# Kernel tuning notes

Hardware: AMD Instinct MI355X
Metric: run time of the kernel (lower is better)

## Reference

```python
import jax, jax.numpy as jnp
import numpy as np

B, S, D = 4, 4096, 128

def setup_inputs() -> dict:
    key = jax.random.key(0)
    kx, kq, kk, kv = jax.random.split(key, 4)
    x = jax.random.normal(kx, (B, S, D), dtype=jnp.float32)
    Wq = jax.random.normal(kq, (D, D), dtype=jnp.float32) * (1.0 / np.sqrt(D))
    Wk = jax.random.normal(kk, (D, D), dtype=jnp.float32) * (1.0 / np.sqrt(D))
    Wv = jax.random.normal(kv, (D, D), dtype=jnp.float32) * (1.0 / np.sqrt(D))
    return {"x": x, "Wq": Wq, "Wk": Wk, "Wv": Wv}

def reference(x, Wq, Wk, Wv):
    b, s, d = x.shape
    # nn.Linear(bias=False): y = x @ W.T
    q = jnp.einsum('bsd,ed->bse', x, Wq)
    k = jnp.einsum('bsd,ed->bse', x, Wk)
    v = jnp.einsum('bsd,ed->bse', x, Wv)
    scores = jnp.einsum('bqd,bkd->bqk', q, k) / jnp.sqrt(jnp.float32(d))
    causal = jnp.tril(jnp.ones((s, s), dtype=bool))  # [s,s]
    scores = jnp.where(causal, scores, jnp.float32(-jnp.inf))
    weights = jax.nn.softmax(scores.astype(jnp.float32), axis=-1)
    out = jnp.einsum('bqk,bkd->bqd', weights, v)
    return out  # dropout is identity in eval / p=0
```

## Files before the change

kernel.cpp:

```cpp
#include <hip/hip_runtime.h>
#include <hip/hip_bf16.h>
#include <math.h>

typedef __attribute__((ext_vector_type(8))) short short8;
typedef __attribute__((ext_vector_type(4))) float f32x4;
typedef __attribute__((ext_vector_type(4))) float float4v;
typedef __attribute__((ext_vector_type(4))) unsigned short ushort4v;

#define B_ 4
#define S_ 4096
#define D_ 128

#define CHUNKS_PER_BATCH 288
#define NSLOT (B_ * CHUNKS_PER_BATCH)

__device__ __forceinline__ unsigned short f2bf(float f) {
    union { float f; unsigned u; } v; v.f = f;
    unsigned r = v.u + 0x7FFFu + ((v.u >> 16) & 1u);
    return (unsigned short)(r >> 16);
}
__device__ __forceinline__ float bf2f(unsigned short h) {
    union { unsigned u; float f; } v; v.u = ((unsigned)h) << 16;
    return v.f;
}

__global__ void wconv_kernel(const float* __restrict__ Wq,
                             const float* __restrict__ Wk,
                             const float* __restrict__ Wv,
                             unsigned short* __restrict__ Wb) {
    int i = blockIdx.x * 256 + threadIdx.x;
    if (i >= 3 * 16384) return;
    const float* s = (i < 16384) ? Wq : (i < 32768 ? Wk : Wv);
    Wb[i] = f2bf(s[i & 16383]);
}

__global__ __launch_bounds__(256) void qkv_kernel(const float* __restrict__ X,
                                                  const unsigned short* __restrict__ Wb,
                                                  unsigned short* __restrict__ Qb,
                                                  unsigned short* __restrict__ Kb,
                                                  unsigned short* __restrict__ Vt) {
    __shared__ __align__(16) unsigned short Xb[64 * 128];
    const int tid = threadIdx.x;
    const int r0 = blockIdx.x * 64;
    const int grp = blockIdx.y;

    const float4v* src = reinterpret_cast<const float4v*>(X + (long)r0 * 128);
    #pragma unroll
    for (int it = 0; it < 8; ++it) {
        int idx = it * 256 + tid;
        float4v v = src[idx];
        ushort4v p;
        p[0] = f2bf(v[0]); p[1] = f2bf(v[1]); p[2] = f2bf(v[2]); p[3] = f2bf(v[3]);
        *reinterpret_cast<ushort4v*>(&Xb[idx * 4]) = p;
    }
    __syncthreads();

    const int lane = tid & 63, w = tid >> 6;
    const int l16 = lane & 15, g = lane >> 4;

    short8 a[4];
    #pragma unroll
    for (int kb = 0; kb < 4; ++kb)
        a[kb] = *reinterpret_cast<const short8*>(&Xb[(w * 16 + l16) * 128 + kb * 32 + g * 8]);

    #pragma unroll
    for (int ct = 0; ct < 8; ++ct) {
        const int e = ct * 16 + l16;
        const int c = grp * 128 + e;
        f32x4 acc = {0.f, 0.f, 0.f, 0.f};
        #pragma unroll
        for (int kb = 0; kb < 4; ++kb) {
            short8 bf = *reinterpret_cast<const short8*>(Wb + (long)c * 128 + kb * 32 + g * 8);
            acc = __builtin_amdgcn_mfma_f32_16x16x32_bf16(a[kb], bf, acc, 0, 0, 0);
        }
        const int row0 = r0 + w * 16 + g * 4;
        if (grp == 0) {
            #pragma unroll
            for (int r = 0; r < 4; ++r) Qb[(long)(row0 + r) * 128 + e] = f2bf(acc[r]);
        } else if (grp == 1) {
            #pragma unroll
            for (int r = 0; r < 4; ++r) Kb[(long)(row0 + r) * 128 + e] = f2bf(acc[r]);
        } else {
            const int bb = row0 >> 12, ss = row0 & 4095;
            ushort4v p;
            p[0] = f2bf(acc[0]); p[1] = f2bf(acc[1]); p[2] = f2bf(acc[2]); p[3] = f2bf(acc[3]);
            *reinterpret_cast<ushort4v*>(&Vt[((long)bb * 128 + e) * 4096 + ss]) = p;
        }
    }
}

__global__ __launch_bounds__(256) void attn_kernel(const unsigned short* __restrict__ Qb,
                                                   const unsigned short* __restrict__ Kb,
                                                   const unsigned short* __restrict__ Vt,
                                                   unsigned short* __restrict__ Opart,
                                                   float* __restrict__ Mpart,
                                                   float* __restrict__ Lpart) {
    __shared__ __align__(16) unsigned char lds[40960];

    const int tid = threadIdx.x;
    const int lane = tid & 63, w = tid >> 6;
    const int l16 = lane & 15, g = lane >> 4;

    const int bidx = (int)blockIdx.x;
    const int b = bidx / CHUNKS_PER_BATCH;
    const int rr = bidx - b * CHUNKS_PER_BATCH;
    int gg = 0;
    while (4 * (gg + 1) * (gg + 2) <= rr) ++gg;
    const int j = rr - 4 * gg * (gg + 1);
    const int qt = 8 * gg + j / (gg + 1);
    const int c = j % (gg + 1);
    const int slot = bidx;

    const unsigned short* Qbase = Qb + (long)b * S_ * D_;
    const unsigned short* Kbase = Kb + (long)b * S_ * D_;
    const unsigned short* Vbase = Vt + (long)b * D_ * S_;

    const int qrow_f = qt * 64 + w * 16 + l16;
    short8 qf[4];
    #pragma unroll
    for (int kb = 0; kb < 4; ++kb)
        qf[kb] = *reinterpret_cast<const short8*>(Qbase + (long)qrow_f * 128 + kb * 32 + g * 8);

    f32x4 o[8];
    #pragma unroll
    for (int dt = 0; dt < 8; ++dt) o[dt] = (f32x4){0.f, 0.f, 0.f, 0.f};
    float m[4], lsum[4];
    int myrow[4];
    #pragma unroll
    for (int r = 0; r < 4; ++r) {
        m[r] = -INFINITY; lsum[r] = 0.f;
        myrow[r] = qt * 64 + w * 16 + g * 4 + r;
    }

    const float scale = 0.08838834764831845f;
    const int kt0 = c * 8;
    const int ktend = min(kt0 + 7, qt);

    for (int kt = kt0; kt <= ktend; ++kt) {
        #pragma unroll
        for (int it = 0; it < 4; ++it) {
            int ch = it * 256 + tid;
            int row = ch >> 4, cd = ch & 15;
            short8 vk = *reinterpret_cast<const short8*>(Kbase + (long)(kt * 64 + row) * 128 + cd * 8);
            int byt = (row * 256 + cd * 16) ^ ((row & 7) << 4);
            *reinterpret_cast<short8*>(lds + byt) = vk;

            int rowd = ch >> 3, ckv = ch & 7;
            short8 vv = *reinterpret_cast<const short8*>(Vbase + (long)rowd * 4096 + kt * 64 + ckv * 8);
            int bytv = (rowd * 128 + ckv * 16) ^ ((rowd & 7) << 4);
            *reinterpret_cast<short8*>(lds + 16384 + bytv) = vv;
        }
        __syncthreads();

        f32x4 s[4];
        #pragma unroll
        for (int ct = 0; ct < 4; ++ct) {
            s[ct] = (f32x4){0.f, 0.f, 0.f, 0.f};
            const int kvl = ct * 16 + l16;
            #pragma unroll
            for (int kb = 0; kb < 4; ++kb) {
                int byt = (kvl * 256 + kb * 64 + g * 16) ^ ((kvl & 7) << 4);
                short8 kf = *reinterpret_cast<const short8*>(lds + byt);
                s[ct] = __builtin_amdgcn_mfma_f32_16x16x32_bf16(qf[kb], kf, s[ct], 0, 0, 0);
            }
        }

        const bool diag = (kt == qt);
        float rmax[4] = {-1e30f, -1e30f, -1e30f, -1e30f};
        #pragma unroll
        for (int ct = 0; ct < 4; ++ct) {
            #pragma unroll
            for (int r = 0; r < 4; ++r) {
                float sv = s[ct][r] * scale;
                if (diag && (kt * 64 + ct * 16 + l16 > myrow[r])) sv = -1e30f;
                s[ct][r] = sv;
                rmax[r] = fmaxf(rmax[r], sv);
            }
        }
        #pragma unroll
        for (int off = 1; off < 16; off <<= 1) {
            #pragma unroll
            for (int r = 0; r < 4; ++r) rmax[r] = fmaxf(rmax[r], __shfl_xor(rmax[r], off, 64));
        }
        float al[4], rsum[4];
        #pragma unroll
        for (int r = 0; r < 4; ++r) {
            float mn = fmaxf(m[r], rmax[r]);
            al[r] = __expf(m[r] - mn);
            m[r] = mn;
            rsum[r] = 0.f;
        }
        #pragma unroll
        for (int ct = 0; ct < 4; ++ct) {
            #pragma unroll
            for (int r = 0; r < 4; ++r) {
                float p = __expf(s[ct][r] - m[r]);
                s[ct][r] = p;
                rsum[r] += p;
            }
        }
        #pragma unroll
        for (int off = 1; off < 16; off <<= 1) {
            #pragma unroll
            for (int r = 0; r < 4; ++r) rsum[r] += __shfl_xor(rsum[r], off, 64);
        }
        #pragma unroll
        for (int r = 0; r < 4; ++r) lsum[r] = lsum[r] * al[r] + rsum[r];
        #pragma unroll
        for (int dt = 0; dt < 8; ++dt) {
            #pragma unroll
            for (int r = 0; r < 4; ++r) o[dt][r] *= al[r];
        }

        unsigned char* Pw = lds + 32768 + w * 2048;
        #pragma unroll
        for (int ct = 0; ct < 4; ++ct) {
            #pragma unroll
            for (int r = 0; r < 4; ++r) {
                int pr = g * 4 + r, pc = ct * 16 + l16;
                int byt = (pr * 128 + pc * 2) ^ ((pr & 7) << 4);
                *reinterpret_cast<unsigned short*>(Pw + byt) = f2bf(s[ct][r]);
            }
        }

        #pragma unroll
        for (int kvb = 0; kvb < 2; ++kvb) {
            int pbyt = (l16 * 128 + kvb * 64 + g * 16) ^ ((l16 & 7) << 4);
            short8 pf = *reinterpret_cast<const short8*>(Pw + pbyt);
            #pragma unroll
            for (int dt = 0; dt < 8; ++dt) {
                int d = dt * 16 + l16;
                int vbyt = (d * 128 + kvb * 64 + g * 16) ^ ((d & 7) << 4);
                short8 vf = *reinterpret_cast<const short8*>(lds + 16384 + vbyt);
                o[dt] = __builtin_amdgcn_mfma_f32_16x16x32_bf16(pf, vf, o[dt], 0, 0, 0);
            }
        }
        __syncthreads();
    }

    unsigned short* Op = Opart + (long)slot * 8192;
    #pragma unroll
    for (int dt = 0; dt < 8; ++dt) {
        #pragma unroll
        for (int r = 0; r < 4; ++r) {
            Op[(w * 16 + g * 4 + r) * 128 + dt * 16 + l16] = f2bf(o[dt][r]);
        }
    }
    if (l16 == 0) {
        #pragma unroll
        for (int r = 0; r < 4; ++r) {
            Mpart[(long)slot * 64 + w * 16 + g * 4 + r] = m[r];
            Lpart[(long)slot * 64 + w * 16 + g * 4 + r] = lsum[r];
        }
    }
}

__global__ __launch_bounds__(256) void combine_kernel(const unsigned short* __restrict__ Opart,
                                                      const float* __restrict__ Mpart,
                                                      const float* __restrict__ Lpart,
                                                      float* __restrict__ out) {
    __shared__ float coeff[8][64];
    __shared__ float invL[64];

    const int qt = blockIdx.x, b = blockIdx.y;
    const int gg = qt >> 3;
    const int nc = gg + 1;
    const int slot0 = b * CHUNKS_PER_BATCH + 4 * gg * (gg + 1) + (qt - 8 * gg) * nc;

    const int tid = threadIdx.x;
    if (tid < 64) {
        float mg = -INFINITY;
        for (int c = 0; c < nc; ++c)
            mg = fmaxf(mg, Mpart[(long)(slot0 + c) * 64 + tid]);
        float L = 0.f;
        for (int c = 0; c < nc; ++c) {
            float co = __expf(Mpart[(long)(slot0 + c) * 64 + tid] - mg);
            coeff[c][tid] = co;
            L += co * Lpart[(long)(slot0 + c) * 64 + tid];
        }
        invL[tid] = 1.f / L;
    }
    __syncthreads();

    #pragma unroll
    for (int it = 0; it < 4; ++it) {
        const int e0 = (it * 256 + tid) * 8;
        const int r = e0 >> 7;
        float acc[8];
        #pragma unroll
        for (int k = 0; k < 8; ++k) acc[k] = 0.f;
        for (int c = 0; c < nc; ++c) {
            short8 v = *reinterpret_cast<const short8*>(Opart + (long)(slot0 + c) * 8192 + e0);
            const float co = coeff[c][r];
            #pragma unroll
            for (int k = 0; k < 8; ++k)
                acc[k] += co * bf2f((unsigned short)v[k]);
        }
        const float s = invL[r];
        float4v o0, o1;
        o0[0] = acc[0] * s; o0[1] = acc[1] * s; o0[2] = acc[2] * s; o0[3] = acc[3] * s;
        o1[0] = acc[4] * s; o1[1] = acc[5] * s; o1[2] = acc[6] * s; o1[3] = acc[7] * s;
        float* dst = out + ((long)b * S_ + qt * 64) * 128 + e0;
        *reinterpret_cast<float4v*>(dst) = o0;
        *reinterpret_cast<float4v*>(dst + 4) = o1;
    }
}

extern "C" void kernel_launch(void* const* d_in, const int* in_sizes, int n_in,
                              void* d_out, int out_size, void* d_ws, size_t ws_size,
                              hipStream_t stream) {
    (void)in_sizes; (void)n_in; (void)out_size; (void)ws_size;
    const float* x  = (const float*)d_in[0];
    const float* Wq = (const float*)d_in[1];
    const float* Wk = (const float*)d_in[2];
    const float* Wv = (const float*)d_in[3];
    float* out = (float*)d_out;

    char* ws = (char*)d_ws;
    const size_t MB4 = (size_t)16384 * 128 * 2;
    unsigned short* Qb = (unsigned short*)(ws);
    unsigned short* Kb = (unsigned short*)(ws + MB4);
    unsigned short* Vt = (unsigned short*)(ws + 2 * MB4);
    unsigned short* Wb = (unsigned short*)(ws + 3 * MB4);
    unsigned short* Opart = (unsigned short*)(ws + 3 * MB4 + (1 << 20));
    float* Mpart = (float*)(ws + 3 * MB4 + (1 << 20) + (size_t)NSLOT * 8192 * 2);
    float* Lpart = Mpart + (size_t)NSLOT * 64;

    wconv_kernel<<<192, 256, 0, stream>>>(Wq, Wk, Wv, Wb);
    qkv_kernel<<<dim3(256, 3), 256, 0, stream>>>(x, Wb, Qb, Kb, Vt);
    attn_kernel<<<NSLOT, 256, 0, stream>>>(Qb, Kb, Vt, Opart, Mpart, Lpart);
    combine_kernel<<<dim3(64, 4), 256, 0, stream>>>(Opart, Mpart, Lpart, out);
}
```

Before: 160.0 us.

## Prefetch next K/V tile into registers, drop QKV LDS staging, split combine blocks

The attention kernel now loads the next K/V tile into registers while the current tile's MFMAs run, then writes it to LDS between barriers. It also adds a min-blocks-per-CU launch bound of 3. The QKV projection loads X straight from global into MFMA fragments instead of staging through LDS. The combine kernel is split into four times as many blocks, each covering 16 rows, to raise parallelism. The prefetch adds register pressure and an extra barrier per iteration, and the launch bound may force spills.

```diff
diff --git a/kernel.cpp b/kernel.cpp
--- a/kernel.cpp
+++ b/kernel.cpp
@@ -39,29 +39,30 @@
                                                   unsigned short* __restrict__ Qb,
                                                   unsigned short* __restrict__ Kb,
                                                   unsigned short* __restrict__ Vt) {
-    __shared__ __align__(16) unsigned short Xb[64 * 128];
     const int tid = threadIdx.x;
+    const int lane = tid & 63, w = tid >> 6;
+    const int l16 = lane & 15, g = lane >> 4;
     const int r0 = blockIdx.x * 64;
     const int grp = blockIdx.y;
 
-    const float4v* src = reinterpret_cast<const float4v*>(X + (long)r0 * 128);
-    #pragma unroll
-    for (int it = 0; it < 8; ++it) {
-        int idx = it * 256 + tid;
-        float4v v = src[idx];
-        ushort4v p;
-        p[0] = f2bf(v[0]); p[1] = f2bf(v[1]); p[2] = f2bf(v[2]); p[3] = f2bf(v[3]);
-        *reinterpret_cast<ushort4v*>(&Xb[idx * 4]) = p;
-    }
-    __syncthreads();
-
-    const int lane = tid & 63, w = tid >> 6;
-    const int l16 = lane & 15, g = lane >> 4;
-
+    const int row = r0 + w * 16 + l16;
+    const float* xr = X + (long)row * 128;
+    float4v x0[4], x1[4];
+    #pragma unroll
+    for (int kb = 0; kb < 4; ++kb) {
+        x0[kb] = *reinterpret_cast<const float4v*>(xr + kb * 32 + g * 8);
+        x1[kb] = *reinterpret_cast<const float4v*>(xr + kb * 32 + g * 8 + 4);
+    }
     short8 a[4];
     #pragma unroll
-    for (int kb = 0; kb < 4; ++kb)
-        a[kb] = *reinterpret_cast<const short8*>(&Xb[(w * 16 + l16) * 128 + kb * 32 + g * 8]);
+    for (int kb = 0; kb < 4; ++kb) {
+        short8 t;
+        t[0] = f2bf(x0[kb][0]); t[1] = f2bf(x0[kb][1]);
+        t[2] = f2bf(x0[kb][2]); t[3] = f2bf(x0[kb][3]);
+        t[4] = f2bf(x1[kb][0]); t[5] = f2bf(x1[kb][1]);
+        t[6] = f2bf(x1[kb][2]); t[7] = f2bf(x1[kb][3]);
+        a[kb] = t;
+    }
 
     #pragma unroll
     for (int ct = 0; ct < 8; ++ct) {
@@ -89,12 +90,12 @@
     }
 }
 
-__global__ __launch_bounds__(256) void attn_kernel(const unsigned short* __restrict__ Qb,
-                                                   const unsigned short* __restrict__ Kb,
-                                                   const unsigned short* __restrict__ Vt,
-                                                   unsigned short* __restrict__ Opart,
-                                                   float* __restrict__ Mpart,
-                                                   float* __restrict__ Lpart) {
+__global__ __launch_bounds__(256, 3) void attn_kernel(const unsigned short* __restrict__ Qb,
+                                                      const unsigned short* __restrict__ Kb,
+                                                      const unsigned short* __restrict__ Vt,
+                                                      unsigned short* __restrict__ Opart,
+                                                      float* __restrict__ Mpart,
+                                                      float* __restrict__ Lpart) {
     __shared__ __align__(16) unsigned char lds[40960];
 
     const int tid = threadIdx.x;
@@ -136,21 +137,45 @@
     const int kt0 = c * 8;
     const int ktend = min(kt0 + 7, qt);
 
+    const int kch = tid, krow0 = kch >> 2, kcd = kch & 3;
+    (void)kch; (void)krow0; (void)kcd;
+
+    short8 kR[4], vR[4];
+    int kbyt[4], vbyt[4];
+    const unsigned short* kaddr[4];
+    const unsigned short* vaddr[4];
+    #pragma unroll
+    for (int it = 0; it < 4; ++it) {
+        int ch = it * 256 + tid;
+        int row = ch >> 4, cd = ch & 15;
+        kaddr[it] = Kbase + (long)row * 128 + cd * 8;
+        kbyt[it] = (row * 256 + cd * 16) ^ ((row & 7) << 4);
+        int rowd = ch >> 3, ckv = ch & 7;
+        vaddr[it] = Vbase + (long)rowd * 4096 + ckv * 8;
+        vbyt[it] = 16384 + ((rowd * 128 + ckv * 16) ^ ((rowd & 7) << 4));
+    }
+
+    #pragma unroll
+    for (int it = 0; it < 4; ++it) {
+        kR[it] = *reinterpret_cast<const short8*>(kaddr[it] + (long)kt0 * 64 * 128);
+        vR[it] = *reinterpret_cast<const short8*>(vaddr[it] + kt0 * 64);
+    }
+    #pragma unroll
+    for (int it = 0; it < 4; ++it) {
+        *reinterpret_cast<short8*>(lds + kbyt[it]) = kR[it];
+        *reinterpret_cast<short8*>(lds + vbyt[it]) = vR[it];
+    }
+    __syncthreads();
+
     for (int kt = kt0; kt <= ktend; ++kt) {
-        #pragma unroll
-        for (int it = 0; it < 4; ++it) {
-            int ch = it * 256 + tid;
-            int row = ch >> 4, cd = ch & 15;
-            short8 vk = *reinterpret_cast<const short8*>(Kbase + (long)(kt * 64 + row) * 128 + cd * 8);
-            int byt = (row * 256 + cd * 16) ^ ((row & 7) << 4);
-            *reinterpret_cast<short8*>(lds + byt) = vk;
-
-            int rowd = ch >> 3, ckv = ch & 7;
-            short8 vv = *reinterpret_cast<const short8*>(Vbase + (long)rowd * 4096 + kt * 64 + ckv * 8);
-            int bytv = (rowd * 128 + ckv * 16) ^ ((rowd & 7) << 4);
-            *reinterpret_cast<short8*>(lds + 16384 + bytv) = vv;
-        }
-        __syncthreads();
+        const bool more = (kt < ktend);
+        if (more) {
+            #pragma unroll
+            for (int it = 0; it < 4; ++it) {
+                kR[it] = *reinterpret_cast<const short8*>(kaddr[it] + (long)(kt + 1) * 64 * 128);
+                vR[it] = *reinterpret_cast<const short8*>(vaddr[it] + (kt + 1) * 64);
+            }
+        }
 
         f32x4 s[4];
         #pragma unroll
@@ -230,12 +255,21 @@
             #pragma unroll
             for (int dt = 0; dt < 8; ++dt) {
                 int d = dt * 16 + l16;
-                int vbyt = (d * 128 + kvb * 64 + g * 16) ^ ((d & 7) << 4);
-                short8 vf = *reinterpret_cast<const short8*>(lds + 16384 + vbyt);
+                int vbyt2 = 16384 + ((d * 128 + kvb * 64 + g * 16) ^ ((d & 7) << 4));
+                short8 vf = *reinterpret_cast<const short8*>(lds + vbyt2);
                 o[dt] = __builtin_amdgcn_mfma_f32_16x16x32_bf16(pf, vf, o[dt], 0, 0, 0);
             }
         }
-        __syncthreads();
+
+        if (more) {
+            __syncthreads();
+            #pragma unroll
+            for (int it = 0; it < 4; ++it) {
+                *reinterpret_cast<short8*>(lds + kbyt[it]) = kR[it];
+                *reinterpret_cast<short8*>(lds + vbyt[it]) = vR[it];
+            }
+            __syncthreads();
+        }
     }
 
     unsigned short* Op = Opart + (long)slot * 8192;
@@ -259,51 +293,49 @@
                                                       const float* __restrict__ Mpart,
                                                       const float* __restrict__ Lpart,
                                                       float* __restrict__ out) {
-    __shared__ float coeff[8][64];
-    __shared__ float invL[64];
-
-    const int qt = blockIdx.x, b = blockIdx.y;
+    __shared__ float coeff[8][16];
+    __shared__ float invL[16];
+
+    const int qt = blockIdx.x >> 2, qq = blockIdx.x & 3, b = blockIdx.y;
     const int gg = qt >> 3;
     const int nc = gg + 1;
     const int slot0 = b * CHUNKS_PER_BATCH + 4 * gg * (gg + 1) + (qt - 8 * gg) * nc;
+    const int r0 = qq * 16;
 
     const int tid = threadIdx.x;
-    if (tid < 64) {
+    if (tid < 16) {
         float mg = -INFINITY;
         for (int c = 0; c < nc; ++c)
-            mg = fmaxf(mg, Mpart[(long)(slot0 + c) * 64 + tid]);
+            mg = fmaxf(mg, Mpart[(long)(slot0 + c) * 64 + r0 + tid]);
         float L = 0.f;
         for (int c = 0; c < nc; ++c) {
-            float co = __expf(Mpart[(long)(slot0 + c) * 64 + tid] - mg);
+            float co = __expf(Mpart[(long)(slot0 + c) * 64 + r0 + tid] - mg);
             coeff[c][tid] = co;
-            L += co * Lpart[(long)(slot0 + c) * 64 + tid];
+            L += co * Lpart[(long)(slot0 + c) * 64 + r0 + tid];
         }
         invL[tid] = 1.f / L;
     }
     __syncthreads();
 
-    #pragma unroll
-    for (int it = 0; it < 4; ++it) {
-        const int e0 = (it * 256 + tid) * 8;
-        const int r = e0 >> 7;
-        float acc[8];
-        #pragma unroll
-        for (int k = 0; k < 8; ++k) acc[k] = 0.f;
-        for (int c = 0; c < nc; ++c) {
-            short8 v = *reinterpret_cast<const short8*>(Opart + (long)(slot0 + c) * 8192 + e0);
-            const float co = coeff[c][r];
-            #pragma unroll
-            for (int k = 0; k < 8; ++k)
-                acc[k] += co * bf2f((unsigned short)v[k]);
-        }
-        const float s = invL[r];
-        float4v o0, o1;
-        o0[0] = acc[0] * s; o0[1] = acc[1] * s; o0[2] = acc[2] * s; o0[3] = acc[3] * s;
-        o1[0] = acc[4] * s; o1[1] = acc[5] * s; o1[2] = acc[6] * s; o1[3] = acc[7] * s;
-        float* dst = out + ((long)b * S_ + qt * 64) * 128 + e0;
-        *reinterpret_cast<float4v*>(dst) = o0;
-        *reinterpret_cast<float4v*>(dst + 4) = o1;
-    }
+    const int e0 = tid * 8;
+    const int r = e0 >> 7;
+    float acc[8];
+    #pragma unroll
+    for (int k = 0; k < 8; ++k) acc[k] = 0.f;
+    for (int c = 0; c < nc; ++c) {
+        short8 v = *reinterpret_cast<const short8*>(Opart + (long)(slot0 + c) * 8192 + r0 * 128 + e0);
+        const float co = coeff[c][r];
+        #pragma unroll
+        for (int k = 0; k < 8; ++k)
+            acc[k] += co * bf2f((unsigned short)v[k]);
+    }
+    const float s = invL[r];
+    float4v o0, o1;
+    o0[0] = acc[0] * s; o0[1] = acc[1] * s; o0[2] = acc[2] * s; o0[3] = acc[3] * s;
+    o1[0] = acc[4] * s; o1[1] = acc[5] * s; o1[2] = acc[6] * s; o1[3] = acc[7] * s;
+    float* dst = out + ((long)b * S_ + qt * 64 + r0) * 128 + e0;
+    *reinterpret_cast<float4v*>(dst) = o0;
+    *reinterpret_cast<float4v*>(dst + 4) = o1;
 }
 
 extern "C" void kernel_launch(void* const* d_in, const int* in_sizes, int n_in,
@@ -329,5 +361,5 @@
     wconv_kernel<<<192, 256, 0, stream>>>(Wq, Wk, Wv, Wb);
     qkv_kernel<<<dim3(256, 3), 256, 0, stream>>>(x, Wb, Qb, Kb, Vt);
     attn_kernel<<<NSLOT, 256, 0, stream>>>(Qb, Kb, Vt, Opart, Mpart, Lpart);
-    combine_kernel<<<dim3(64, 4), 256, 0, stream>>>(Opart, Mpart, Lpart, out);
-}
+    combine_kernel<<<dim3(256, 4), 256, 0, stream>>>(Opart, Mpart, Lpart, out);
+}
```

New measurement: 212.8 us. 1.33x slower.
